# Kernel tuning notes

Hardware: AMD Instinct MI355X
Metric: run time of the kernel (lower is better)

The kernel has to match this reference:

```python
import jax, jax.numpy as jnp
import numpy as np

B, S, D, H, K = 16, 2048, 1024, 16, 31  # batch, seq, d_model, n_heads, kernel_size


def setup_inputs() -> dict:
    key = jax.random.key(0)
    ks = jax.random.split(key, 6)
    sc = 1.0 / np.sqrt(D)
    return {
        "query_sequences": jax.random.normal(ks[0], (B, S, D), jnp.float32),
        "key_sequences": jax.random.normal(ks[1], (B, S, D), jnp.float32),
        "value_sequences": jax.random.normal(ks[2], (B, S, D), jnp.float32),
        "key_value_sequence_lengths": jax.random.randint(ks[3], (B,), 1, S + 1, jnp.int32),
        "W_q": jax.random.normal(ks[4], (D, H * K), jnp.float32) * sc,  # cast_queries.weight^T
        "b_q": jnp.zeros((H * K,), jnp.float32),                        # cast_queries.bias
        "conv_bias": jnp.zeros((H,), jnp.float32),
    }


def reference(query_sequences, key_sequences, value_sequences,
              key_value_sequence_lengths, W_q, b_q, conv_bias):
    b, s, d = query_sequences.shape
    h = conv_bias.shape[0]
    k = W_q.shape[1] // h
    r = d // h
    # Generate per-position, per-head depthwise filters from the queries.
    weights = (query_sequences @ W_q + b_q).reshape(b, s, h, k)  # (B,S,H,K)
    # Split key channels into heads and reduce within each head -> (B,S,H)
    ksum = key_sequences.reshape(b, s, h, r).sum(axis=-1)
    pad_l = (k - 1) // 2
    pad_r = k - 1 - pad_l
    kpad = jnp.pad(ksum, ((0, 0), (pad_l, pad_r), (0, 0)))  # (B, S+K-1, H)
    # Cross-correlation with per-position filters:
    # out[b,t,h] = sum_j weights[b,t,h,j] * kpad[b, t+j, h]
    out = jnp.zeros((b, s, h), dtype=weights.dtype)
    for j in range(k):  # fixed small kernel loop
        out = out + weights[..., j] * kpad[:, j:j + s, :]
    out = out + conv_bias  # per-head bias
    return out.transpose(0, 2, 1)  # (B, n_heads, S)
```

## Files before the change

kernel.cpp:

```cpp
#include <hip/hip_runtime.h>
#include <hip/hip_bf16.h>

#define BB 16
#define SS 2048
#define DD 1024
#define HH 16
#define KK 31
#define HK 496

typedef float f32x4 __attribute__((ext_vector_type(4)));
typedef __bf16 bf16x8 __attribute__((ext_vector_type(8)));

__device__ __forceinline__ unsigned short f2bf(float x) {
  unsigned u = __float_as_uint(x);
  unsigned r = u + 0x7FFFu + ((u >> 16) & 1u);
  return (unsigned short)(r >> 16);
}

__device__ __forceinline__ void gll16(const void* g, void* l) {
  __builtin_amdgcn_global_load_lds(
      (const __attribute__((address_space(1))) unsigned int*)g,
      (__attribute__((address_space(3))) unsigned int*)l, 16, 0, 0);
}

__global__ void prep_kernel(const float* __restrict__ Wq,
                            unsigned short* __restrict__ Bimg) {
  int idx = blockIdx.x * 256 + threadIdx.x;
  int ks = idx >> 15;
  int rem = idx & 32767;
  int c = rem >> 6;
  int s = (rem >> 3) & 7;
  int e = rem & 7;
  int k8 = s ^ (c & 7);
  int k = ks * 64 + k8 * 8 + e;
  int h = c >> 5, j = c & 31;
  float v = (j < KK) ? Wq[k * HK + h * KK + j] : 0.f;
  Bimg[idx] = f2bf(v);
}

__global__ void ksum_kernel(const float* __restrict__ key,
                            float* __restrict__ ksum) {
  const int row = blockIdx.x;
  const int tid = threadIdx.x;
  const float4 v = reinterpret_cast<const float4*>(key + (size_t)row * DD)[tid];
  float p = v.x + v.y + v.z + v.w;
  p += __shfl_xor(p, 1);
  p += __shfl_xor(p, 2);
  p += __shfl_xor(p, 4);
  p += __shfl_xor(p, 8);
  if ((tid & 15) == 0) ksum[(size_t)row * HH + (tid >> 4)] = p;
}

__global__ __launch_bounds__(512, 2) void mca_kernel(
    const float* __restrict__ q, const float* __restrict__ bq,
    const float* __restrict__ convb, const float* __restrict__ ksum,
    const unsigned short* __restrict__ Bimg, float* __restrict__ out) {
  extern __shared__ char smem[];
  const int tid = threadIdx.x;
  const int wave = tid >> 6, lane = tid & 63;
  const int g = lane >> 4, qq = lane & 15;
  const int wr = wave >> 2, wc = wave & 3;
  const int bid = blockIdx.x;
  const int bb = bid >> 4;
  const int t0 = (bid & 15) << 7;

  char* const bB0 = smem;
  char* const bB1 = smem + 65536;
  char* const bA0 = smem + 131072;
  char* const bA1 = smem + 147456;

  const float* qblk = q + ((size_t)(bb * SS + t0)) * DD;

  f32x4 acc[4][8];
#pragma unroll
  for (int m = 0; m < 4; ++m)
#pragma unroll
    for (int n = 0; n < 8; ++n) acc[m][n] = (f32x4){0.f, 0.f, 0.f, 0.f};

  const int arow0 = tid >> 3;
  const int aslot = tid & 7;
  const int ak8 = aslot ^ (arow0 & 7);

  float4 rA[2][2];

  auto stageB = [&](char* dst, int ks) {
    const char* src = (const char*)Bimg + (size_t)ks * 65536 + wave * 1024 + lane * 16;
    char* d = dst + wave * 1024;
#pragma unroll
    for (int rr = 0; rr < 8; ++rr) gll16(src + rr * 8192, d + rr * 8192);
  };

  auto issueA = [&](int ks) {
#pragma unroll
    for (int rep = 0; rep < 2; ++rep) {
      const float* src = qblk + (size_t)(arow0 + rep * 64) * DD + ks * 64 + ak8 * 8;
      rA[rep][0] = ((const float4*)src)[0];
      rA[rep][1] = ((const float4*)src)[1];
    }
  };

  auto writeA = [&](char* dst) {
#pragma unroll
    for (int rep = 0; rep < 2; ++rep) {
      float f[8] = {rA[rep][0].x, rA[rep][0].y, rA[rep][0].z, rA[rep][0].w,
                    rA[rep][1].x, rA[rep][1].y, rA[rep][1].z, rA[rep][1].w};
      unsigned u[4];
#pragma unroll
      for (int i = 0; i < 4; ++i)
        u[i] = (unsigned)f2bf(f[2 * i]) | ((unsigned)f2bf(f[2 * i + 1]) << 16);
      *reinterpret_cast<uint4*>(dst + (arow0 + rep * 64) * 128 + aslot * 16) =
          make_uint4(u[0], u[1], u[2], u[3]);
    }
  };

  auto computeT = [&](const char* bufA, const char* bufB) {
#pragma unroll
    for (int kk = 0; kk < 2; ++kk) {
      const int x = ((kk * 4 + g) ^ (lane & 7)) * 16;
      bf16x8 af[4], bf[8];
#pragma unroll
      for (int m = 0; m < 4; ++m)
        af[m] = *reinterpret_cast<const bf16x8*>(bufA + (wr * 64 + m * 16 + qq) * 128 + x);
#pragma unroll
      for (int n = 0; n < 8; ++n)
        bf[n] = *reinterpret_cast<const bf16x8*>(bufB + (wc * 128 + n * 16 + qq) * 128 + x);
#pragma unroll
      for (int m = 0; m < 4; ++m)
#pragma unroll
        for (int n = 0; n < 8; ++n)
          acc[m][n] = __builtin_amdgcn_mfma_f32_16x16x32_bf16(af[m], bf[n], acc[m][n], 0, 0, 0);
    }
  };

  issueA(0);
  stageB(bB0, 0);
  writeA(bA0);
  __syncthreads();

  for (int ks = 0; ks < 16; ++ks) {
    char* cA = (ks & 1) ? bA1 : bA0;
    char* cB = (ks & 1) ? bB1 : bB0;
    char* nA = (ks & 1) ? bA0 : bA1;
    char* nB = (ks & 1) ? bB0 : bB1;
    if (ks < 15) {
      issueA(ks + 1);
      stageB(nB, ks + 1);
    }
    computeT(cA, cB);
    if (ks < 15) writeA(nA);
    __syncthreads();
  }

  float bqv[8];
#pragma unroll
  for (int n = 0; n < 8; ++n) {
    int c = wc * 128 + n * 16 + qq;
    int h = c >> 5, j = c & 31;
    bqv[n] = (j < KK) ? bq[h * KK + j] : 0.f;
  }
  float cb[4];
#pragma unroll
  for (int hp = 0; hp < 4; ++hp) cb[hp] = convb[wc * 4 + hp];

  float* kl = reinterpret_cast<float*>(smem);
  for (int i = tid; i < 160 * 16; i += 512) {
    int trow = i >> 4, h = i & 15;
    int t = t0 + trow - 15;
    kl[trow * 17 + h] = (t >= 0 && t < SS) ? ksum[((size_t)bb * SS + t) * HH + h] : 0.f;
  }
  __syncthreads();

#pragma unroll
  for (int m = 0; m < 4; ++m) {
    float part[4][4];
#pragma unroll
    for (int r = 0; r < 4; ++r)
#pragma unroll
      for (int hp = 0; hp < 4; ++hp) part[r][hp] = 0.f;
#pragma unroll
    for (int n = 0; n < 8; ++n) {
      const int hp = n >> 1;
      const int j = (n & 1) * 16 + qq;
      const int h = wc * 4 + hp;
#pragma unroll
      for (int r = 0; r < 4; ++r) {
        const int tl = wr * 64 + m * 16 + g * 4 + r;
        part[r][hp] += (acc[m][n][r] + bqv[n]) * kl[(tl + j) * 17 + h];
      }
    }
#pragma unroll
    for (int r = 0; r < 4; ++r)
#pragma unroll
      for (int hp = 0; hp < 4; ++hp) {
        float v = part[r][hp];
        v += __shfl_xor(v, 1);
        v += __shfl_xor(v, 2);
        v += __shfl_xor(v, 4);
        v += __shfl_xor(v, 8);
        part[r][hp] = v;
      }
    if (qq < 4) {
      const int r = qq;
      const int t = t0 + wr * 64 + m * 16 + g * 4 + r;
#pragma unroll
      for (int hp = 0; hp < 4; ++hp)
        out[((size_t)bb * HH + wc * 4 + hp) * SS + t] = part[r][hp] + cb[hp];
    }
  }
}

extern "C" void kernel_launch(void* const* d_in, const int* in_sizes, int n_in,
                              void* d_out, int out_size, void* d_ws, size_t ws_size,
                              hipStream_t stream) {
  const float* q   = (const float*)d_in[0];
  const float* key = (const float*)d_in[1];
  const float* Wq  = (const float*)d_in[4];
  const float* bq  = (const float*)d_in[5];
  const float* cvb = (const float*)d_in[6];
  float* out = (float*)d_out;

  float* ksum = (float*)d_ws;
  unsigned short* Bimg = (unsigned short*)((char*)d_ws + 2097152);

  hipFuncSetAttribute((const void*)mca_kernel,
                      hipFuncAttributeMaxDynamicSharedMemorySize, 163840);

  prep_kernel<<<2048, 256, 0, stream>>>(Wq, Bimg);
  ksum_kernel<<<BB * SS, 256, 0, stream>>>(key, ksum);
  mca_kernel<<<BB * (SS / 128), 512, 163840, stream>>>(q, bq, cvb, ksum, Bimg, out);
}
```

Baseline: 82.34 us.

## Shrink GEMM tile to 64 rows and K-step 32 for higher occupancy

Retiles the fused projection-plus-convolution kernel. Each block now covers 64 timesteps instead of 128, and the K dimension is stepped 32 at a time instead of 64. Each wave owns a full 64-row by 64-column slice rather than a 64x128 quadrant. The B-image layout drops its XOR swizzle in favour of a k-group-major arrangement, and LDS use falls from 160KB to 72KB so launch bounds allow 4 blocks per CU. The goals are more resident blocks, twice as many blocks in the grid, and fewer accumulator registers. The trade-off is that the B tile is reloaded by twice as many blocks, there are twice as many barrier-separated K iterations, and LDS reads are unswizzled, which may cause bank conflicts.

```diff
diff --git a/kernel.cpp b/kernel.cpp
--- a/kernel.cpp
+++ b/kernel.cpp
@@ -26,13 +26,11 @@
 __global__ void prep_kernel(const float* __restrict__ Wq,
                             unsigned short* __restrict__ Bimg) {
   int idx = blockIdx.x * 256 + threadIdx.x;
-  int ks = idx >> 15;
-  int rem = idx & 32767;
-  int c = rem >> 6;
-  int s = (rem >> 3) & 7;
-  int e = rem & 7;
-  int k8 = s ^ (c & 7);
-  int k = ks * 64 + k8 * 8 + e;
+  int e = idx & 7;
+  int c = (idx >> 3) & 511;
+  int gr = (idx >> 12) & 3;
+  int ks = idx >> 14;
+  int k = ks * 32 + gr * 8 + e;
   int h = c >> 5, j = c & 31;
   float v = (j < KK) ? Wq[k * HK + h * KK + j] : 0.f;
   Bimg[idx] = f2bf(v);
@@ -51,85 +49,67 @@
   if ((tid & 15) == 0) ksum[(size_t)row * HH + (tid >> 4)] = p;
 }
 
-__global__ __launch_bounds__(512, 2) void mca_kernel(
+__global__ __launch_bounds__(512, 4) void mca_kernel(
     const float* __restrict__ q, const float* __restrict__ bq,
     const float* __restrict__ convb, const float* __restrict__ ksum,
     const unsigned short* __restrict__ Bimg, float* __restrict__ out) {
   extern __shared__ char smem[];
   const int tid = threadIdx.x;
-  const int wave = tid >> 6, lane = tid & 63;
+  const int w = tid >> 6, lane = tid & 63;
   const int g = lane >> 4, qq = lane & 15;
-  const int wr = wave >> 2, wc = wave & 3;
   const int bid = blockIdx.x;
-  const int bb = bid >> 4;
-  const int t0 = (bid & 15) << 7;
+  const int bb = bid >> 5;
+  const int t0 = (bid & 31) << 6;
 
   char* const bB0 = smem;
-  char* const bB1 = smem + 65536;
-  char* const bA0 = smem + 131072;
-  char* const bA1 = smem + 147456;
+  char* const bB1 = smem + 32768;
+  char* const bA0 = smem + 65536;
+  char* const bA1 = smem + 69632;
 
   const float* qblk = q + ((size_t)(bb * SS + t0)) * DD;
 
-  f32x4 acc[4][8];
+  f32x4 acc[4][4];
 #pragma unroll
   for (int m = 0; m < 4; ++m)
 #pragma unroll
-    for (int n = 0; n < 8; ++n) acc[m][n] = (f32x4){0.f, 0.f, 0.f, 0.f};
-
-  const int arow0 = tid >> 3;
-  const int aslot = tid & 7;
-  const int ak8 = aslot ^ (arow0 & 7);
-
-  float4 rA[2][2];
+    for (int n = 0; n < 4; ++n) acc[m][n] = (f32x4){0.f, 0.f, 0.f, 0.f};
+
+  const int arow = tid >> 3;
+  const int apart = tid & 7;
+  const int ag = apart >> 1, ah = apart & 1;
+
+  float4 rA;
 
   auto stageB = [&](char* dst, int ks) {
-    const char* src = (const char*)Bimg + (size_t)ks * 65536 + wave * 1024 + lane * 16;
-    char* d = dst + wave * 1024;
-#pragma unroll
-    for (int rr = 0; rr < 8; ++rr) gll16(src + rr * 8192, d + rr * 8192);
+    const char* src = (const char*)Bimg + (size_t)ks * 32768 + w * 1024 + lane * 16;
+    char* d = dst + w * 1024;
+#pragma unroll
+    for (int rr = 0; rr < 4; ++rr) gll16(src + rr * 8192, d + rr * 8192);
   };
 
   auto issueA = [&](int ks) {
-#pragma unroll
-    for (int rep = 0; rep < 2; ++rep) {
-      const float* src = qblk + (size_t)(arow0 + rep * 64) * DD + ks * 64 + ak8 * 8;
-      rA[rep][0] = ((const float4*)src)[0];
-      rA[rep][1] = ((const float4*)src)[1];
-    }
+    rA = *reinterpret_cast<const float4*>(qblk + (size_t)arow * DD + ks * 32 + apart * 4);
   };
 
   auto writeA = [&](char* dst) {
-#pragma unroll
-    for (int rep = 0; rep < 2; ++rep) {
-      float f[8] = {rA[rep][0].x, rA[rep][0].y, rA[rep][0].z, rA[rep][0].w,
-                    rA[rep][1].x, rA[rep][1].y, rA[rep][1].z, rA[rep][1].w};
-      unsigned u[4];
-#pragma unroll
-      for (int i = 0; i < 4; ++i)
-        u[i] = (unsigned)f2bf(f[2 * i]) | ((unsigned)f2bf(f[2 * i + 1]) << 16);
-      *reinterpret_cast<uint4*>(dst + (arow0 + rep * 64) * 128 + aslot * 16) =
-          make_uint4(u[0], u[1], u[2], u[3]);
-    }
+    unsigned u0 = (unsigned)f2bf(rA.x) | ((unsigned)f2bf(rA.y) << 16);
+    unsigned u1 = (unsigned)f2bf(rA.z) | ((unsigned)f2bf(rA.w) << 16);
+    *reinterpret_cast<uint2*>(dst + ag * 1024 + arow * 16 + ah * 8) = make_uint2(u0, u1);
   };
 
   auto computeT = [&](const char* bufA, const char* bufB) {
-#pragma unroll
-    for (int kk = 0; kk < 2; ++kk) {
-      const int x = ((kk * 4 + g) ^ (lane & 7)) * 16;
-      bf16x8 af[4], bf[8];
-#pragma unroll
-      for (int m = 0; m < 4; ++m)
-        af[m] = *reinterpret_cast<const bf16x8*>(bufA + (wr * 64 + m * 16 + qq) * 128 + x);
-#pragma unroll
-      for (int n = 0; n < 8; ++n)
-        bf[n] = *reinterpret_cast<const bf16x8*>(bufB + (wc * 128 + n * 16 + qq) * 128 + x);
-#pragma unroll
-      for (int m = 0; m < 4; ++m)
-#pragma unroll
-        for (int n = 0; n < 8; ++n)
-          acc[m][n] = __builtin_amdgcn_mfma_f32_16x16x32_bf16(af[m], bf[n], acc[m][n], 0, 0, 0);
-    }
+    bf16x8 af[4], bf[4];
+#pragma unroll
+    for (int m = 0; m < 4; ++m)
+      af[m] = *reinterpret_cast<const bf16x8*>(bufA + g * 1024 + (m * 16 + qq) * 16);
+#pragma unroll
+    for (int n = 0; n < 4; ++n)
+      bf[n] = *reinterpret_cast<const bf16x8*>(bufB + g * 8192 + (w * 64 + n * 16 + qq) * 16);
+#pragma unroll
+    for (int m = 0; m < 4; ++m)
+#pragma unroll
+      for (int n = 0; n < 4; ++n)
+        acc[m][n] = __builtin_amdgcn_mfma_f32_16x16x32_bf16(af[m], bf[n], acc[m][n], 0, 0, 0);
   };
 
   issueA(0);
@@ -137,33 +117,31 @@
   writeA(bA0);
   __syncthreads();
 
-  for (int ks = 0; ks < 16; ++ks) {
+  for (int ks = 0; ks < 32; ++ks) {
     char* cA = (ks & 1) ? bA1 : bA0;
     char* cB = (ks & 1) ? bB1 : bB0;
     char* nA = (ks & 1) ? bA0 : bA1;
     char* nB = (ks & 1) ? bB0 : bB1;
-    if (ks < 15) {
+    if (ks < 31) {
       issueA(ks + 1);
       stageB(nB, ks + 1);
     }
     computeT(cA, cB);
-    if (ks < 15) writeA(nA);
+    if (ks < 31) writeA(nA);
     __syncthreads();
   }
 
-  float bqv[8];
-#pragma unroll
-  for (int n = 0; n < 8; ++n) {
-    int c = wc * 128 + n * 16 + qq;
+  float bqv[4];
+#pragma unroll
+  for (int n = 0; n < 4; ++n) {
+    int c = w * 64 + n * 16 + qq;
     int h = c >> 5, j = c & 31;
     bqv[n] = (j < KK) ? bq[h * KK + j] : 0.f;
   }
-  float cb[4];
-#pragma unroll
-  for (int hp = 0; hp < 4; ++hp) cb[hp] = convb[wc * 4 + hp];
+  float cb[2] = {convb[w * 2], convb[w * 2 + 1]};
 
   float* kl = reinterpret_cast<float*>(smem);
-  for (int i = tid; i < 160 * 16; i += 512) {
+  for (int i = tid; i < 96 * 16; i += 512) {
     int trow = i >> 4, h = i & 15;
     int t = t0 + trow - 15;
     kl[trow * 17 + h] = (t >= 0 && t < SS) ? ksum[((size_t)bb * SS + t) * HH + h] : 0.f;
@@ -172,26 +150,27 @@
 
 #pragma unroll
   for (int m = 0; m < 4; ++m) {
-    float part[4][4];
-#pragma unroll
-    for (int r = 0; r < 4; ++r)
-#pragma unroll
-      for (int hp = 0; hp < 4; ++hp) part[r][hp] = 0.f;
-#pragma unroll
-    for (int n = 0; n < 8; ++n) {
+    float part[4][2];
+#pragma unroll
+    for (int r = 0; r < 4; ++r) {
+      part[r][0] = 0.f;
+      part[r][1] = 0.f;
+    }
+#pragma unroll
+    for (int n = 0; n < 4; ++n) {
       const int hp = n >> 1;
       const int j = (n & 1) * 16 + qq;
-      const int h = wc * 4 + hp;
+      const int h = w * 2 + hp;
 #pragma unroll
       for (int r = 0; r < 4; ++r) {
-        const int tl = wr * 64 + m * 16 + g * 4 + r;
+        const int tl = m * 16 + g * 4 + r;
         part[r][hp] += (acc[m][n][r] + bqv[n]) * kl[(tl + j) * 17 + h];
       }
     }
 #pragma unroll
     for (int r = 0; r < 4; ++r)
 #pragma unroll
-      for (int hp = 0; hp < 4; ++hp) {
+      for (int hp = 0; hp < 2; ++hp) {
         float v = part[r][hp];
         v += __shfl_xor(v, 1);
         v += __shfl_xor(v, 2);
@@ -201,10 +180,10 @@
       }
     if (qq < 4) {
       const int r = qq;
-      const int t = t0 + wr * 64 + m * 16 + g * 4 + r;
-#pragma unroll
-      for (int hp = 0; hp < 4; ++hp)
-        out[((size_t)bb * HH + wc * 4 + hp) * SS + t] = part[r][hp] + cb[hp];
+      const int t = t0 + m * 16 + g * 4 + r;
+#pragma unroll
+      for (int hp = 0; hp < 2; ++hp)
+        out[((size_t)bb * HH + w * 2 + hp) * SS + t] = part[r][hp] + cb[hp];
     }
   }
 }
@@ -223,9 +202,9 @@
   unsigned short* Bimg = (unsigned short*)((char*)d_ws + 2097152);
 
   hipFuncSetAttribute((const void*)mca_kernel,
-                      hipFuncAttributeMaxDynamicSharedMemorySize, 163840);
+                      hipFuncAttributeMaxDynamicSharedMemorySize, 73728);
 
   prep_kernel<<<2048, 256, 0, stream>>>(Wq, Bimg);
   ksum_kernel<<<BB * SS, 256, 0, stream>>>(key, ksum);
-  mca_kernel<<<BB * (SS / 128), 512, 163840, stream>>>(q, bq, cvb, ksum, Bimg, out);
-}
+  mca_kernel<<<BB * (SS / 64), 512, 73728, stream>>>(q, bq, cvb, ksum, Bimg, out);
+}
```

Result: slower. 89.16 us (+8.3%).
